# Optimization experiments

Hardware: AMD Instinct MI355X
Metric: run time of the kernel (lower is better)

Reference implementation:

```python
import jax, jax.numpy as jnp
import numpy as np

N = 32768
E = 8           # num_submodules (4x2 grid)
HID = 256       # hidden_dim
POS_DIM = 63    # 3*(1+2*10)
DIR_DIM = 27    # 3*(1+2*4)
APP_DIM = 48
IN_DIM = POS_DIM + APP_DIM        # 111
SKIP_IN = HID + IN_DIM            # 367
COL_IN = HID + DIR_DIM            # 283
COL_HID = HID // 2                # 128
NUM_APP = 1000

SCENE = np.array([-100.0, -100.0, -10.0, 100.0, 100.0, 50.0], np.float32)
_margin = (1.0 - 0.8) / 2.0       # (1 - foreground_ratio)/2
_rng = SCENE[3:] - SCENE[:3]
FG_LO = SCENE[:3] + _rng * _margin
FG_HI = SCENE[3:] - _rng * _margin

def _centroids():
    xs = np.linspace(-100.0, 100.0, 3)   # grid_cols + 1
    ys = np.linspace(-100.0, 100.0, 5)   # grid_rows + 1
    zc = (-10.0 + 50.0) / 2.0
    cs = []
    for i in range(4):
        for j in range(2):
            cs.append([(xs[j] + xs[j + 1]) / 2.0, (ys[i] + ys[i + 1]) / 2.0, zc])
    return np.asarray(cs, np.float32)
CENTROIDS = _centroids()  # [E,3]

def posenc(x, max_log2, num_freqs):
    freqs = (2.0 ** np.linspace(0.0, max_log2, num_freqs)).astype(np.float32)
    parts = [x]
    for f in freqs:
        parts.append(jnp.sin(f * x))
        parts.append(jnp.cos(f * x))
    return jnp.concatenate(parts, axis=-1)

def setup_inputs() -> dict:
    key = jax.random.key(0)
    ks = jax.random.split(key, 24)
    lo, hi = jnp.asarray(SCENE[:3]), jnp.asarray(SCENE[3:])
    points = jax.random.uniform(ks[0], (N, 3), jnp.float32) * (hi - lo) + lo
    vd = jax.random.normal(ks[1], (N, 3), jnp.float32)
    viewdirs = vd / jnp.linalg.norm(vd, axis=-1, keepdims=True)
    appearance_idx = jax.random.randint(ks[2], (N,), 0, NUM_APP, jnp.int32)
    s = 0.02
    p = lambda k, shape: jax.random.normal(k, shape, jnp.float32) * s
    return {
        'points': points, 'viewdirs': viewdirs, 'appearance_idx': appearance_idx,
        'app_embed': p(ks[3], (E, NUM_APP, APP_DIM)),
        'W0': p(ks[4], (E, IN_DIM, HID)),      'b0': p(ks[5], (E, HID)),
        'W_pre': p(ks[6], (E, 3, HID, HID)),   'b_pre': p(ks[7], (E, 3, HID)),
        'Wskip': p(ks[8], (E, SKIP_IN, HID)),  'bskip': p(ks[9], (E, HID)),
        'W_post': p(ks[10], (E, 3, HID, HID)), 'b_post': p(ks[11], (E, 3, HID)),
        'Wd': p(ks[12], (E, HID, 1)),          'bd': p(ks[13], (E, 1)),
        'Wf': p(ks[14], (E, HID, HID)),        'bf': p(ks[15], (E, HID)),
        'Wc1': p(ks[16], (E, COL_IN, COL_HID)),'bc1': p(ks[17], (E, COL_HID)),
        'Wc2': p(ks[18], (E, COL_HID, 3)),     'bc2': p(ks[19], (E, 3)),
    }

def _forward(points, viewdirs, appearance_idx, app_embed, W0, b0, W_pre, b_pre,
             Wskip, bskip, W_post, b_post, Wd, bd, Wf, bf, Wc1, bc1, Wc2, bc2):
    n = points.shape[0]
    cen = jnp.asarray(CENTROIDS)
    fg = jnp.all((points >= jnp.asarray(FG_LO)) & (points <= jnp.asarray(FG_HI)), axis=-1)  # [N]
    # nearest-centroid routing (argmin of L2 == argmin of squared L2)
    expert = jnp.argmin(jnp.sum((points[:, None, :] - cen[None]) ** 2, axis=-1), axis=1)  # [N]
    pe = posenc(points, 10.0, 10)                              # [N,63]
    app = app_embed[:, appearance_idx, :]                      # [E,N,48] per-expert embedding lookup
    x0 = jnp.concatenate([jnp.broadcast_to(pe[None], (E, n, POS_DIM)), app], axis=-1)  # [E,N,111]
    x = jax.nn.relu(jnp.einsum('eni,eih->enh', x0, W0) + b0[:, None])
    for i in range(3):  # linear layers 1..3
        x = jax.nn.relu(jnp.einsum('enh,ehk->enk', x, W_pre[:, i]) + b_pre[:, i][:, None])
    x = jnp.concatenate([x, x0], axis=-1)                      # skip connection at layer 4
    x = jax.nn.relu(jnp.einsum('eni,eih->enh', x, Wskip) + bskip[:, None])
    for i in range(3):  # linear layers 5..7
        x = jax.nn.relu(jnp.einsum('enh,ehk->enk', x, W_post[:, i]) + b_post[:, i][:, None])
    density = jax.nn.relu(jnp.einsum('enh,eho->eno', x, Wd) + bd[:, None])   # [E,N,1]
    feat = jnp.einsum('enh,ehk->enk', x, Wf) + bf[:, None]                   # feature_head (no relu)
    de = posenc(viewdirs, 4.0, 4)                              # [N,27]
    cin = jnp.concatenate([feat, jnp.broadcast_to(de[None], (E, n, DIR_DIM))], axis=-1)  # [E,N,283]
    h = jax.nn.relu(jnp.einsum('eni,eih->enh', cin, Wc1) + bc1[:, None])
    color = jax.nn.sigmoid(jnp.einsum('enh,eho->eno', h, Wc2) + bc2[:, None])  # [E,N,3]
    rows = jnp.arange(n)
    d = jnp.where(fg[:, None], density[expert, rows], 0.0)     # combine: pick routed expert, zero bg
    c = jnp.where(fg[:, None], color[expert, rows], 0.0)
    return d, c

def reference(points, viewdirs, appearance_idx, app_embed, W0, b0, W_pre, b_pre,
              Wskip, bskip, W_post, b_post, Wd, bd, Wf, bf, Wc1, bc1, Wc2, bc2):
    return _forward(points, viewdirs, appearance_idx, app_embed, W0, b0, W_pre, b_pre,
                    Wskip, bskip, W_post, b_post, Wd, bd, Wf, bf, Wc1, bc1, Wc2, bc2)
```

## Files before the change

### kernel.cpp

```cpp
#include <hip/hip_runtime.h>
#include <hip/hip_bf16.h>
#include <math.h>

typedef __bf16 bf16;
typedef __bf16 bf16x4 __attribute__((ext_vector_type(4)));
typedef __bf16 bf16x8 __attribute__((ext_vector_type(8)));
typedef float  f32x4  __attribute__((ext_vector_type(4)));

#define N_PTS 32768

__global__ void k_point(const float* __restrict__ pts, float* __restrict__ out,
                        int* __restrict__ counts, unsigned short* __restrict__ idxlist) {
    __shared__ int lcnt[8], lbase[8];
    int t = threadIdx.x;
    int n = blockIdx.x * 256 + t;
    if (t < 8) lcnt[t] = 0;
    __syncthreads();
    float px = pts[3*n+0], py = pts[3*n+1], pz = pts[3*n+2];
    int e = 0; float best = 3.4e38f;
    #pragma unroll
    for (int i = 0; i < 4; ++i)
        #pragma unroll
        for (int j = 0; j < 2; ++j) {
            float cx = j ? 50.f : -50.f, cy = -75.f + 50.f * i;
            float dx = px - cx, dy = py - cy, dz = pz - 20.f;
            float d = dx*dx + dy*dy + dz*dz;
            if (d < best) { best = d; e = i*2 + j; }
        }
    bool fg = (px >= -80.f && px <= 80.f && py >= -80.f && py <= 80.f &&
               pz >= -4.f  && pz <= 44.f);
    int slot = -1;
    if (fg) {
        slot = atomicAdd(&lcnt[e], 1);
    } else {
        out[n] = 0.f;
        out[N_PTS + 3*n + 0] = 0.f;
        out[N_PTS + 3*n + 1] = 0.f;
        out[N_PTS + 3*n + 2] = 0.f;
    }
    __syncthreads();
    if (t < 8) lbase[t] = atomicAdd(&counts[t], lcnt[t]);
    __syncthreads();
    if (slot >= 0) idxlist[e * N_PTS + lbase[e] + slot] = (unsigned short)n;
}

__global__ void k_tp(const float* __restrict__ s0, const float* __restrict__ s1,
                     const float* __restrict__ s2, const float* __restrict__ s3,
                     const float* __restrict__ s4, const float* __restrict__ s5,
                     bf16* __restrict__ d0, bf16* __restrict__ d1, bf16* __restrict__ d2,
                     bf16* __restrict__ d3, bf16* __restrict__ d4, bf16* __restrict__ d5,
                     const float* __restrict__ pts, float* __restrict__ out,
                     int* __restrict__ counts, unsigned short* __restrict__ idxlist) {
    int t = threadIdx.x;
    if (blockIdx.y == 6) {
        __shared__ int lcnt[8], lbase[8];
        if (blockIdx.x >= N_PTS / 256) return;
        int n = blockIdx.x * 256 + t;
        if (t < 8) lcnt[t] = 0;
        __syncthreads();
        float px = pts[3*n+0], py = pts[3*n+1], pz = pts[3*n+2];
        int e = 0; float best = 3.4e38f;
        #pragma unroll
        for (int i = 0; i < 4; ++i)
            #pragma unroll
            for (int j = 0; j < 2; ++j) {
                float cx = j ? 50.f : -50.f, cy = -75.f + 50.f * i;
                float dx = px - cx, dy = py - cy, dz = pz - 20.f;
                float d = dx*dx + dy*dy + dz*dz;
                if (d < best) { best = d; e = i*2 + j; }
            }
        bool fg = (px >= -80.f && px <= 80.f && py >= -80.f && py <= 80.f &&
                   pz >= -4.f  && pz <= 44.f);
        int slot = -1;
        if (fg) {
            slot = atomicAdd(&lcnt[e], 1);
        } else {
            out[n] = 0.f;
            out[N_PTS + 3*n + 0] = 0.f;
            out[N_PTS + 3*n + 1] = 0.f;
            out[N_PTS + 3*n + 2] = 0.f;
        }
        __syncthreads();
        if (t < 8) lbase[t] = atomicAdd(&counts[t], lcnt[t]);
        __syncthreads();
        if (slot >= 0) idxlist[e * N_PTS + lbase[e] + slot] = (unsigned short)n;
        return;
    }
    __shared__ bf16 tile[64 * 68];
    const float* src; bf16* dst; int K, Nn, Kpad, Eg;
    switch (blockIdx.y) {
        case 0:  src = s0; dst = d0; K = 111; Nn = 256; Kpad = 128; Eg = 8;  break;
        case 1:  src = s1; dst = d1; K = 256; Nn = 256; Kpad = 256; Eg = 24; break;
        case 2:  src = s2; dst = d2; K = 367; Nn = 256; Kpad = 384; Eg = 8;  break;
        case 3:  src = s3; dst = d3; K = 256; Nn = 256; Kpad = 256; Eg = 24; break;
        case 4:  src = s4; dst = d4; K = 256; Nn = 256; Kpad = 256; Eg = 8;  break;
        default: src = s5; dst = d5; K = 283; Nn = 128; Kpad = 288; Eg = 8;  break;
    }
    int ktiles = (Kpad + 63) / 64, ntiles = Nn / 64;
    int b = blockIdx.x;
    if (b >= Eg * ktiles * ntiles) return;
    int eg = b / (ktiles * ntiles), rem = b % (ktiles * ntiles);
    int kt = rem / ntiles, nt = rem % ntiles;
    #pragma unroll
    for (int r = 0; r < 4; ++r) {
        int idx = r * 256 + t;
        int kl = idx >> 4, nl4 = (idx & 15) * 4;
        int kg = kt * 64 + kl, ng = nt * 64 + nl4;
        bf16x4 v = (bf16x4){(bf16)0.f, (bf16)0.f, (bf16)0.f, (bf16)0.f};
        if (kg < K) {
            f32x4 f = *(const f32x4*)(src + ((size_t)(eg * K + kg)) * Nn + ng);
            v[0] = (bf16)f[0]; v[1] = (bf16)f[1]; v[2] = (bf16)f[2]; v[3] = (bf16)f[3];
        }
        *(bf16x4*)(&tile[kl * 68 + nl4]) = v;
    }
    __syncthreads();
    #pragma unroll
    for (int i = 0; i < 2; ++i) {
        int idx = i * 256 + t;
        int ng_l = idx >> 3, kq = idx & 7;
        int kg = kt * 64 + kq * 8, ng = nt * 64 + ng_l;
        if (kg < Kpad) {
            bf16x8 v;
            #pragma unroll
            for (int j = 0; j < 8; ++j) v[j] = tile[(kq * 8 + j) * 68 + ng_l];
            size_t off = ((size_t)(ng >> 5) * (Kpad >> 5) + (size_t)(kg >> 5)) * 1024
                       + (size_t)((ng >> 4) & 1) * 512
                       + (size_t)((kg >> 3) & 3) * 128
                       + (size_t)(ng & 15) * 8;
            *(bf16x8*)(dst + (size_t)eg * Nn * Kpad + off) = v;
        }
    }
}

__device__ __forceinline__ f32x4 mfma16(bf16x8 a, bf16x8 b, f32x4 c) {
    return __builtin_amdgcn_mfma_f32_16x16x32_bf16(a, b, c, 0, 0, 0);
}

__device__ __forceinline__ void zacc(f32x4 acc[4][2]) {
    #pragma unroll
    for (int i = 0; i < 4; ++i)
        #pragma unroll
        for (int j = 0; j < 2; ++j) acc[i][j] = (f32x4){0.f, 0.f, 0.f, 0.f};
}

template<int NS, int KPAD>
__device__ __forceinline__ void gemm_p(f32x4 acc[4][2], const bf16* A, int astr,
                                       const bf16* __restrict__ Wt, int wk0,
                                       int nbase, int l16, int quad, int lane) {
    const bf16* bp = Wt + ((size_t)(nbase >> 5) * (KPAD >> 5) + (size_t)(wk0 >> 5)) * 1024
                   + (size_t)lane * 8;
    #pragma unroll
    for (int s = 0; s < NS; ++s) {
        int kA = s * 32 + quad * 8;
        bf16x8 b0 = *(const bf16x8*)(bp + s * 1024);
        bf16x8 b1 = *(const bf16x8*)(bp + s * 1024 + 512);
        #pragma unroll
        for (int m = 0; m < 4; ++m) {
            bf16x8 a = *(const bf16x8*)(A + (size_t)(m * 16 + l16) * astr + kA);
            acc[m][0] = mfma16(a, b0, acc[m][0]);
            acc[m][1] = mfma16(a, b1, acc[m][1]);
        }
    }
}

template<int NS, bool GUARD>
__device__ __forceinline__ void gemm_g(f32x4 acc[4][2], const bf16* A, int astr,
                                       const float* __restrict__ W, int ldn, int wk0, int Klim,
                                       int nbase, int l16, int quad) {
    #pragma unroll
    for (int s = 0; s < NS; ++s) {
        int kA = s * 32 + quad * 8;
        #pragma unroll
        for (int nt = 0; nt < 2; ++nt) {
            int n = nbase + nt * 16 + l16;
            const float* wp = W + (size_t)(wk0 + kA) * ldn + n;
            bf16x8 b;
            #pragma unroll
            for (int j = 0; j < 8; ++j) {
                float wv = 0.f;
                if (!GUARD || (wk0 + kA + j < Klim)) wv = wp[(size_t)j * ldn];
                b[j] = (bf16)wv;
            }
            #pragma unroll
            for (int m = 0; m < 4; ++m) {
                bf16x8 a = *(const bf16x8*)(A + (size_t)(m * 16 + l16) * astr + kA);
                acc[m][nt] = mfma16(a, b, acc[m][nt]);
            }
        }
    }
}

__device__ __forceinline__ void epi(f32x4 acc[4][2], const float* bias, bool dorelu,
                                    bf16* dst, int dstr, int nbase, int l16, int quad) {
    #pragma unroll
    for (int nt = 0; nt < 2; ++nt) {
        float bv = bias[nbase + nt * 16 + l16];
        #pragma unroll
        for (int m = 0; m < 4; ++m) {
            #pragma unroll
            for (int r = 0; r < 4; ++r) {
                float v = acc[m][nt][r] + bv;
                v = fminf(fmaxf(v, -64.f), 64.f);
                if (dorelu) v = fmaxf(v, 0.f);
                dst[(size_t)(m * 16 + quad * 4 + r) * dstr + nbase + nt * 16 + l16] = (bf16)v;
            }
        }
    }
}

template<bool PACKED>
__global__ __launch_bounds__(512, 2)
void k_main(const int* __restrict__ counts, const unsigned short* __restrict__ idxlist,
            const float* __restrict__ pts, const float* __restrict__ dirs,
            const float* __restrict__ app_embed, const int* __restrict__ aidx,
            const float* __restrict__ W0, const float* __restrict__ b0,
            const float* __restrict__ W_pre, const float* __restrict__ b_pre,
            const float* __restrict__ Wskip, const float* __restrict__ bskip,
            const float* __restrict__ W_post, const float* __restrict__ b_post,
            const float* __restrict__ Wd, const float* __restrict__ bd,
            const float* __restrict__ Wf, const float* __restrict__ bf_,
            const float* __restrict__ Wc1, const float* __restrict__ bc1,
            const float* __restrict__ Wc2, const float* __restrict__ bc2,
            const bf16* __restrict__ wt0, const bf16* __restrict__ wtpre,
            const bf16* __restrict__ wtskip, const bf16* __restrict__ wtpost,
            const bf16* __restrict__ wtf, const bf16* __restrict__ wtc1,
            float* __restrict__ out) {
    extern __shared__ char smem[];
    bf16* xaA  = (bf16*)smem;
    bf16* xaB  = xaA + 64 * 264;
    bf16* x0l  = xaB + 64 * 264;
    bf16* del  = x0l + 64 * 136;
    int*  gidx = (int*)(del + 64 * 48);
    int*  aid  = gidx + 64;

    const int e    = blockIdx.x & 7;
    const int tile = blockIdx.x >> 3;
    const int cnt  = counts[e];
    if (tile * 64 >= cnt) return;
    const int t = threadIdx.x;
    const int lane = t & 63, wv = t >> 6;
    const int l16 = lane & 15, quad = lane >> 4;
    const int nbase = wv * 32;

    if (t < 64) {
        int i = tile * 64 + t;
        int g = (i < cnt) ? (int)idxlist[e * N_PTS + i] : -1;
        gidx[t] = g;
        aid[t]  = (g >= 0) ? aidx[g] : 0;
    }
    __syncthreads();
    {
        int row = t >> 3, c0 = t & 7, g = gidx[row];
        float p0 = 0.f, p1 = 0.f, p2 = 0.f, q0 = 0.f, q1 = 0.f, q2 = 0.f;
        if (g >= 0) {
            p0 = pts[3*g+0];  p1 = pts[3*g+1];  p2 = pts[3*g+2];
            q0 = dirs[3*g+0]; q1 = dirs[3*g+1]; q2 = dirs[3*g+2];
        }
        int ai = aid[row];
        #pragma unroll
        for (int i = 0; i < 16; ++i) {
            int col = c0 + 8 * i;
            float v = 0.f;
            if (g >= 0 && col < 111) {
                if (col < 3) {
                    v = (col == 0) ? p0 : (col == 1) ? p1 : p2;
                } else if (col < 63) {
                    int q = col - 3, fi = q / 6, d = q % 6, ax = (d < 3) ? d : (d - 3);
                    float p = (ax == 0) ? p0 : (ax == 1) ? p1 : p2;
                    float f = (float)exp2((double)fi * (10.0 / 9.0));
                    v = (d < 3) ? sinf(f * p) : cosf(f * p);
                } else {
                    v = app_embed[((size_t)(e * 1000 + ai)) * 48 + (col - 63)];
                }
            }
            x0l[row * 136 + col] = (bf16)v;
        }
        #pragma unroll
        for (int i = 0; i < 4; ++i) {
            int col = c0 + 8 * i;
            float v = 0.f;
            if (g >= 0 && col < 27) {
                if (col < 3) {
                    v = (col == 0) ? q0 : (col == 1) ? q1 : q2;
                } else {
                    int q = col - 3, fi = q / 6, d = q % 6, ax = (d < 3) ? d : (d - 3);
                    float p = (ax == 0) ? q0 : (ax == 1) ? q1 : q2;
                    float f = (float)exp2((double)fi * (4.0 / 3.0));
                    v = (d < 3) ? sinf(f * p) : cosf(f * p);
                }
            }
            del[row * 48 + col] = (bf16)v;
        }
    }
    __syncthreads();

    f32x4 acc[4][2];
    zacc(acc);
    if (PACKED) gemm_p<4, 128>(acc, x0l, 136, wt0 + (size_t)e * 32768, 0, nbase, l16, quad, lane);
    else        gemm_g<4, true>(acc, x0l, 136, W0 + (size_t)e * 28416, 256, 0, 111, nbase, l16, quad);
    epi(acc, b0 + e * 256, true, xaA, 264, nbase, l16, quad);
    __syncthreads();
    #pragma unroll
    for (int i = 0; i < 3; ++i) {
        const bf16* src = (i & 1) ? xaB : xaA;
        bf16*       dst = (i & 1) ? xaA : xaB;
        zacc(acc);
        if (PACKED) gemm_p<8, 256>(acc, src, 264, wtpre + (size_t)(e * 3 + i) * 65536, 0, nbase, l16, quad, lane);
        else        gemm_g<8, false>(acc, src, 264, W_pre + (size_t)(e * 3 + i) * 65536, 256, 0, 256, nbase, l16, quad);
        epi(acc, b_pre + (e * 3 + i) * 256, true, dst, 264, nbase, l16, quad);
        __syncthreads();
    }
    zacc(acc);
    if (PACKED) {
        gemm_p<8, 384>(acc, xaB, 264, wtskip + (size_t)e * 98304, 0,   nbase, l16, quad, lane);
        gemm_p<4, 384>(acc, x0l, 136, wtskip + (size_t)e * 98304, 256, nbase, l16, quad, lane);
    } else {
        gemm_g<8, false>(acc, xaB, 264, Wskip + (size_t)e * 93952, 256, 0,   367, nbase, l16, quad);
        gemm_g<4, true >(acc, x0l, 136, Wskip + (size_t)e * 93952, 256, 256, 367, nbase, l16, quad);
    }
    epi(acc, bskip + e * 256, true, xaA, 264, nbase, l16, quad);
    __syncthreads();
    #pragma unroll
    for (int i = 0; i < 3; ++i) {
        const bf16* src = (i & 1) ? xaB : xaA;
        bf16*       dst = (i & 1) ? xaA : xaB;
        zacc(acc);
        if (PACKED) gemm_p<8, 256>(acc, src, 264, wtpost + (size_t)(e * 3 + i) * 65536, 0, nbase, l16, quad, lane);
        else        gemm_g<8, false>(acc, src, 264, W_post + (size_t)(e * 3 + i) * 65536, 256, 0, 256, nbase, l16, quad);
        epi(acc, b_post + (e * 3 + i) * 256, true, dst, 264, nbase, l16, quad);
        __syncthreads();
    }
    {
        int m = t >> 3, p = t & 7;
        const bf16*  xr = xaB + (size_t)m * 264;
        const float* wd = Wd + e * 256;
        float s = 0.f;
        #pragma unroll
        for (int kk = 0; kk < 32; ++kk) s += (float)xr[p * 32 + kk] * wd[p * 32 + kk];
        s += __shfl_down(s, 4, 8);
        s += __shfl_down(s, 2, 8);
        s += __shfl_down(s, 1, 8);
        if (p == 0) {
            int g = gidx[m];
            if (g >= 0) out[g] = fminf(fmaxf(s + bd[e], 0.f), 64.f);
        }
    }
    zacc(acc);
    if (PACKED) gemm_p<8, 256>(acc, xaB, 264, wtf + (size_t)e * 65536, 0, nbase, l16, quad, lane);
    else        gemm_g<8, false>(acc, xaB, 264, Wf + (size_t)e * 65536, 256, 0, 256, nbase, l16, quad);
    epi(acc, bf_ + e * 256, false, xaA, 264, nbase, l16, quad);
    __syncthreads();
    if (wv < 4) {
        zacc(acc);
        if (PACKED) {
            gemm_p<8, 288>(acc, xaA, 264, wtc1 + (size_t)e * 36864, 0,   nbase, l16, quad, lane);
            gemm_p<1, 288>(acc, del, 48,  wtc1 + (size_t)e * 36864, 256, nbase, l16, quad, lane);
        } else {
            gemm_g<8, false>(acc, xaA, 264, Wc1 + (size_t)e * 36224, 128, 0,   283, nbase, l16, quad);
            gemm_g<1, true >(acc, del, 48,  Wc1 + (size_t)e * 36224, 128, 256, 283, nbase, l16, quad);
        }
        epi(acc, bc1 + e * 128, true, xaB, 264, nbase, l16, quad);
    }
    __syncthreads();
    if (t < 192) {
        int m = t & 63, c = t >> 6;
        int g = gidx[m];
        if (g >= 0) {
            const bf16*  xr = xaB + (size_t)m * 264;
            const float* w  = Wc2 + e * 384 + c;
            float s = 0.f;
            for (int k = 0; k < 128; ++k) s += (float)xr[k] * w[k * 3];
            s += bc2[e * 3 + c];
            s = fminf(fmaxf(s, -30.f), 30.f);
            out[N_PTS + 3 * g + c] = 1.f / (1.f + expf(-s));
        }
    }
}

extern "C" void kernel_launch(void* const* d_in, const int* in_sizes, int n_in,
                              void* d_out, int out_size, void* d_ws, size_t ws_size,
                              hipStream_t stream) {
    const float* points    = (const float*)d_in[0];
    const float* viewdirs  = (const float*)d_in[1];
    const int*   aidx      = (const int*)  d_in[2];
    const float* app_embed = (const float*)d_in[3];
    const float* W0        = (const float*)d_in[4];
    const float* b0        = (const float*)d_in[5];
    const float* W_pre     = (const float*)d_in[6];
    const float* b_pre     = (const float*)d_in[7];
    const float* Wskip     = (const float*)d_in[8];
    const float* bskip     = (const float*)d_in[9];
    const float* W_post    = (const float*)d_in[10];
    const float* b_post    = (const float*)d_in[11];
    const float* Wd        = (const float*)d_in[12];
    const float* bd        = (const float*)d_in[13];
    const float* Wf        = (const float*)d_in[14];
    const float* bf_       = (const float*)d_in[15];
    const float* Wc1       = (const float*)d_in[16];
    const float* bc1       = (const float*)d_in[17];
    const float* Wc2       = (const float*)d_in[18];
    const float* bc2       = (const float*)d_in[19];
    float* out = (float*)d_out;
    (void)in_sizes; (void)n_in; (void)out_size;

    char* ws = (char*)d_ws;
    size_t off = 0;
    auto alloc = [&](size_t bytes) -> void* {
        void* p = ws + off;
        off += (bytes + 255) & ~(size_t)255;
        return p;
    };
    int*            counts  = (int*)            alloc(8 * 4);
    unsigned short* idxlist = (unsigned short*) alloc((size_t)8 * N_PTS * 2);
    bf16* wt0    = (bf16*)alloc((size_t)8  * 256 * 128 * 2);
    bf16* wtpre  = (bf16*)alloc((size_t)24 * 256 * 256 * 2);
    bf16* wtskip = (bf16*)alloc((size_t)8  * 256 * 384 * 2);
    bf16* wtpost = (bf16*)alloc((size_t)24 * 256 * 256 * 2);
    bf16* wtf    = (bf16*)alloc((size_t)8  * 256 * 256 * 2);
    bf16* wtc1   = (bf16*)alloc((size_t)8  * 128 * 288 * 2);
    const bool packed = (off <= ws_size);

    const size_t SMEM = (size_t)(64*264 + 64*264 + 64*136 + 64*48) * 2 + 64 * 4 * 2;

    hipMemsetAsync(counts, 0, 8 * sizeof(int), stream);
    #define MAIN_ARGS counts, idxlist, points, viewdirs, app_embed, aidx, \
        W0, b0, W_pre, b_pre, Wskip, bskip, W_post, b_post, Wd, bd, Wf, bf_, \
        Wc1, bc1, Wc2, bc2, wt0, wtpre, wtskip, wtpost, wtf, wtc1, out
    if (packed) {
        hipLaunchKernelGGL(k_tp, dim3(384, 7), dim3(256), 0, stream,
                           W0, W_pre, Wskip, W_post, Wf, Wc1,
                           wt0, wtpre, wtskip, wtpost, wtf, wtc1,
                           points, out, counts, idxlist);
        hipLaunchKernelGGL(k_main<true>,  dim3(8 * (N_PTS / 64)), dim3(512), SMEM, stream, MAIN_ARGS);
    } else {
        hipLaunchKernelGGL(k_point, dim3(N_PTS / 256), dim3(256), 0, stream,
                           points, out, counts, idxlist);
        hipLaunchKernelGGL(k_main<false>, dim3(8 * (N_PTS / 64)), dim3(512), SMEM, stream, MAIN_ARGS);
    }
    #undef MAIN_ARGS
}
```

Before: 187.0 us.

## Use 16 waves per block with one 16-column MFMA tile per wave

Doubles the block from 512 to 1024 threads and gives each wave a 16-column slice of N instead of 32. Each wave now holds 4 accumulators instead of 8 and issues half the MFMAs per A-fragment load. The featurization, density dot-product and color layers are re-split to match the new thread count. The goal is more waves in flight to hide LDS and global latency, at the cost of loading each A fragment twice as often across waves and tighter register limits from the launch bounds.

Measured after the change: 179.1 us. 4.2% less time.

```diff
diff --git a/kernel.cpp b/kernel.cpp
--- a/kernel.cpp
+++ b/kernel.cpp
@@ -136,80 +136,70 @@
     return __builtin_amdgcn_mfma_f32_16x16x32_bf16(a, b, c, 0, 0, 0);
 }
 
-__device__ __forceinline__ void zacc(f32x4 acc[4][2]) {
-    #pragma unroll
-    for (int i = 0; i < 4; ++i)
-        #pragma unroll
-        for (int j = 0; j < 2; ++j) acc[i][j] = (f32x4){0.f, 0.f, 0.f, 0.f};
+__device__ __forceinline__ void zacc(f32x4 acc[4]) {
+    #pragma unroll
+    for (int i = 0; i < 4; ++i) acc[i] = (f32x4){0.f, 0.f, 0.f, 0.f};
 }
 
 template<int NS, int KPAD>
-__device__ __forceinline__ void gemm_p(f32x4 acc[4][2], const bf16* A, int astr,
+__device__ __forceinline__ void gemm_p(f32x4 acc[4], const bf16* A, int astr,
                                        const bf16* __restrict__ Wt, int wk0,
                                        int nbase, int l16, int quad, int lane) {
     const bf16* bp = Wt + ((size_t)(nbase >> 5) * (KPAD >> 5) + (size_t)(wk0 >> 5)) * 1024
-                   + (size_t)lane * 8;
+                   + (size_t)((nbase >> 4) & 1) * 512 + (size_t)lane * 8;
     #pragma unroll
     for (int s = 0; s < NS; ++s) {
         int kA = s * 32 + quad * 8;
-        bf16x8 b0 = *(const bf16x8*)(bp + s * 1024);
-        bf16x8 b1 = *(const bf16x8*)(bp + s * 1024 + 512);
+        bf16x8 b = *(const bf16x8*)(bp + s * 1024);
         #pragma unroll
         for (int m = 0; m < 4; ++m) {
             bf16x8 a = *(const bf16x8*)(A + (size_t)(m * 16 + l16) * astr + kA);
-            acc[m][0] = mfma16(a, b0, acc[m][0]);
-            acc[m][1] = mfma16(a, b1, acc[m][1]);
+            acc[m] = mfma16(a, b, acc[m]);
         }
     }
 }
 
 template<int NS, bool GUARD>
-__device__ __forceinline__ void gemm_g(f32x4 acc[4][2], const bf16* A, int astr,
+__device__ __forceinline__ void gemm_g(f32x4 acc[4], const bf16* A, int astr,
                                        const float* __restrict__ W, int ldn, int wk0, int Klim,
                                        int nbase, int l16, int quad) {
     #pragma unroll
     for (int s = 0; s < NS; ++s) {
         int kA = s * 32 + quad * 8;
-        #pragma unroll
-        for (int nt = 0; nt < 2; ++nt) {
-            int n = nbase + nt * 16 + l16;
-            const float* wp = W + (size_t)(wk0 + kA) * ldn + n;
-            bf16x8 b;
-            #pragma unroll
-            for (int j = 0; j < 8; ++j) {
-                float wv = 0.f;
-                if (!GUARD || (wk0 + kA + j < Klim)) wv = wp[(size_t)j * ldn];
-                b[j] = (bf16)wv;
-            }
-            #pragma unroll
-            for (int m = 0; m < 4; ++m) {
-                bf16x8 a = *(const bf16x8*)(A + (size_t)(m * 16 + l16) * astr + kA);
-                acc[m][nt] = mfma16(a, b, acc[m][nt]);
-            }
-        }
-    }
-}
-
-__device__ __forceinline__ void epi(f32x4 acc[4][2], const float* bias, bool dorelu,
+        int n = nbase + l16;
+        const float* wp = W + (size_t)(wk0 + kA) * ldn + n;
+        bf16x8 b;
+        #pragma unroll
+        for (int j = 0; j < 8; ++j) {
+            float wv = 0.f;
+            if (!GUARD || (wk0 + kA + j < Klim)) wv = wp[(size_t)j * ldn];
+            b[j] = (bf16)wv;
+        }
+        #pragma unroll
+        for (int m = 0; m < 4; ++m) {
+            bf16x8 a = *(const bf16x8*)(A + (size_t)(m * 16 + l16) * astr + kA);
+            acc[m] = mfma16(a, b, acc[m]);
+        }
+    }
+}
+
+__device__ __forceinline__ void epi(f32x4 acc[4], const float* bias, bool dorelu,
                                     bf16* dst, int dstr, int nbase, int l16, int quad) {
-    #pragma unroll
-    for (int nt = 0; nt < 2; ++nt) {
-        float bv = bias[nbase + nt * 16 + l16];
-        #pragma unroll
-        for (int m = 0; m < 4; ++m) {
-            #pragma unroll
-            for (int r = 0; r < 4; ++r) {
-                float v = acc[m][nt][r] + bv;
-                v = fminf(fmaxf(v, -64.f), 64.f);
-                if (dorelu) v = fmaxf(v, 0.f);
-                dst[(size_t)(m * 16 + quad * 4 + r) * dstr + nbase + nt * 16 + l16] = (bf16)v;
-            }
+    float bv = bias[nbase + l16];
+    #pragma unroll
+    for (int m = 0; m < 4; ++m) {
+        #pragma unroll
+        for (int r = 0; r < 4; ++r) {
+            float v = acc[m][r] + bv;
+            v = fminf(fmaxf(v, -64.f), 64.f);
+            if (dorelu) v = fmaxf(v, 0.f);
+            dst[(size_t)(m * 16 + quad * 4 + r) * dstr + nbase + l16] = (bf16)v;
         }
     }
 }
 
 template<bool PACKED>
-__global__ __launch_bounds__(512, 2)
+__global__ __launch_bounds__(1024, 4)
 void k_main(const int* __restrict__ counts, const unsigned short* __restrict__ idxlist,
             const float* __restrict__ pts, const float* __restrict__ dirs,
             const float* __restrict__ app_embed, const int* __restrict__ aidx,
@@ -240,7 +230,7 @@
     const int t = threadIdx.x;
     const int lane = t & 63, wv = t >> 6;
     const int l16 = lane & 15, quad = lane >> 4;
-    const int nbase = wv * 32;
+    const int nbase = wv * 16;
 
     if (t < 64) {
         int i = tile * 64 + t;
@@ -250,7 +240,7 @@
     }
     __syncthreads();
     {
-        int row = t >> 3, c0 = t & 7, g = gidx[row];
+        int row = t >> 4, c0 = t & 15, g = gidx[row];
         float p0 = 0.f, p1 = 0.f, p2 = 0.f, q0 = 0.f, q1 = 0.f, q2 = 0.f;
         if (g >= 0) {
             p0 = pts[3*g+0];  p1 = pts[3*g+1];  p2 = pts[3*g+2];
@@ -258,8 +248,8 @@
         }
         int ai = aid[row];
         #pragma unroll
-        for (int i = 0; i < 16; ++i) {
-            int col = c0 + 8 * i;
+        for (int i = 0; i < 8; ++i) {
+            int col = c0 + 16 * i;
             float v = 0.f;
             if (g >= 0 && col < 111) {
                 if (col < 3) {
@@ -276,8 +266,8 @@
             x0l[row * 136 + col] = (bf16)v;
         }
         #pragma unroll
-        for (int i = 0; i < 4; ++i) {
-            int col = c0 + 8 * i;
+        for (int i = 0; i < 2; ++i) {
+            int col = c0 + 16 * i;
             float v = 0.f;
             if (g >= 0 && col < 27) {
                 if (col < 3) {
@@ -294,7 +284,7 @@
     }
     __syncthreads();
 
-    f32x4 acc[4][2];
+    f32x4 acc[4];
     zacc(acc);
     if (PACKED) gemm_p<4, 128>(acc, x0l, 136, wt0 + (size_t)e * 32768, 0, nbase, l16, quad, lane);
     else        gemm_g<4, true>(acc, x0l, 136, W0 + (size_t)e * 28416, 256, 0, 111, nbase, l16, quad);
@@ -331,15 +321,16 @@
         __syncthreads();
     }
     {
-        int m = t >> 3, p = t & 7;
+        int m = t >> 4, p = t & 15;
         const bf16*  xr = xaB + (size_t)m * 264;
         const float* wd = Wd + e * 256;
         float s = 0.f;
         #pragma unroll
-        for (int kk = 0; kk < 32; ++kk) s += (float)xr[p * 32 + kk] * wd[p * 32 + kk];
-        s += __shfl_down(s, 4, 8);
-        s += __shfl_down(s, 2, 8);
-        s += __shfl_down(s, 1, 8);
+        for (int kk = 0; kk < 16; ++kk) s += (float)xr[p * 16 + kk] * wd[p * 16 + kk];
+        s += __shfl_down(s, 8, 16);
+        s += __shfl_down(s, 4, 16);
+        s += __shfl_down(s, 2, 16);
+        s += __shfl_down(s, 1, 16);
         if (p == 0) {
             int g = gidx[m];
             if (g >= 0) out[g] = fminf(fmaxf(s + bd[e], 0.f), 64.f);
@@ -350,7 +341,7 @@
     else        gemm_g<8, false>(acc, xaB, 264, Wf + (size_t)e * 65536, 256, 0, 256, nbase, l16, quad);
     epi(acc, bf_ + e * 256, false, xaA, 264, nbase, l16, quad);
     __syncthreads();
-    if (wv < 4) {
+    if (wv < 8) {
         zacc(acc);
         if (PACKED) {
             gemm_p<8, 288>(acc, xaA, 264, wtc1 + (size_t)e * 36864, 0,   nbase, l16, quad, lane);
@@ -431,11 +422,11 @@
                            W0, W_pre, Wskip, W_post, Wf, Wc1,
                            wt0, wtpre, wtskip, wtpost, wtf, wtc1,
                            points, out, counts, idxlist);
-        hipLaunchKernelGGL(k_main<true>,  dim3(8 * (N_PTS / 64)), dim3(512), SMEM, stream, MAIN_ARGS);
+        hipLaunchKernelGGL(k_main<true>,  dim3(8 * (N_PTS / 64)), dim3(1024), SMEM, stream, MAIN_ARGS);
     } else {
         hipLaunchKernelGGL(k_point, dim3(N_PTS / 256), dim3(256), 0, stream,
                            points, out, counts, idxlist);
-        hipLaunchKernelGGL(k_main<false>, dim3(8 * (N_PTS / 64)), dim3(512), SMEM, stream, MAIN_ARGS);
+        hipLaunchKernelGGL(k_main<false>, dim3(8 * (N_PTS / 64)), dim3(1024), SMEM, stream, MAIN_ARGS);
     }
     #undef MAIN_ARGS
 }
```
